# Kernel tuning notes

Measured on AMD Instinct MI355X. Metric: run time of the kernel, lower is better.

Reference implementation:

```python
import jax, jax.numpy as jnp
import numpy as np

N_NODES = 50000

def gcn_conv(x, src, dst, W, b, n_nodes):
    # PyG GCNConv: add self-loops, symmetric normalization D^-1/2 (A+I) D^-1/2, then bias
    loop = jnp.arange(n_nodes)
    s = jnp.concatenate([src, loop])
    d = jnp.concatenate([dst, loop])
    deg = jax.ops.segment_sum(jnp.ones(s.shape[0], x.dtype), d, num_segments=n_nodes)
    dinv = jnp.where(deg > 0, jax.lax.rsqrt(deg), 0.0)
    norm = dinv[s] * dinv[d]                      # [E+N]
    h = x @ W                                      # [N, out]
    msg = h[s] * norm[:, None]                     # gather + scale
    out = jax.ops.segment_sum(msg, d, num_segments=n_nodes)  # scatter-add
    return out + b

def setup_inputs() -> dict:
    key = jax.random.key(0)
    ks = jax.random.split(key, 8)
    x = jax.random.normal(ks[0], (N_NODES, 128), jnp.float32)
    edge_index = jax.random.randint(ks[1], (2, 800000), 0, N_NODES)
    def glorot(k, fan_in, fan_out):
        lim = np.sqrt(6.0 / (fan_in + fan_out)).astype(np.float32)
        return jax.random.uniform(k, (fan_in, fan_out), jnp.float32, -lim, lim)
    return {
        "x": x,
        "edge_index": edge_index,
        "conv_w1": glorot(ks[2], 128, 64), "conv_b1": jnp.zeros((64,), jnp.float32),
        "conv_w2": glorot(ks[3], 64, 64),  "conv_b2": jnp.zeros((64,), jnp.float32),
        "fc_w1": glorot(ks[4], 64, 32),    "fc_b1": jnp.zeros((32,), jnp.float32),
        "fc_w2": glorot(ks[5], 32, 1),     "fc_b2": jnp.zeros((1,), jnp.float32),
    }

def reference(x, edge_index, conv_w1, conv_b1, conv_w2, conv_b2, fc_w1, fc_b1, fc_w2, fc_b2):
    src, dst = edge_index[0], edge_index[1]
    h = jnp.tanh(gcn_conv(x, src, dst, conv_w1, conv_b1, N_NODES))
    h = jnp.tanh(gcn_conv(h, src, dst, conv_w2, conv_b2, N_NODES))
    h = jnp.tanh(h @ fc_w1 + fc_b1)  # dropout is identity at inference
    return h @ fc_w2 + fc_b2          # [N, 1]
```

## Files before the change

kernel.cpp:

```cpp
#include <hip/hip_runtime.h>
#include <math.h>

#define TPB 256
#define NBK_MAX 512
#define CAP 4096
#define FILL_CAP 4096
#define SC_CH 16
#define DMAX 64

typedef short bf16x8 __attribute__((ext_vector_type(8)));
typedef float f32x4 __attribute__((ext_vector_type(4)));

__device__ __forceinline__ unsigned short rne_bf16(float f) {
  unsigned u = __float_as_uint(f);
  return (unsigned short)((u + 0x7fffu + ((u >> 16) & 1u)) >> 16);
}
__device__ __forceinline__ float bf16_f(unsigned short v) {
  return __uint_as_float((unsigned)v << 16);
}
__device__ __forceinline__ float blo(unsigned u) { return __uint_as_float(u << 16); }
__device__ __forceinline__ float bhi(unsigned u) { return __uint_as_float(u & 0xffff0000u); }
__device__ __forceinline__ float ftanh(float x) {
  float xc = fminf(fmaxf(x, -15.f), 15.f);
  float e = __expf(2.f * xc);
  return (e - 1.f) * __builtin_amdgcn_rcpf(e + 1.f);
}

__global__ __launch_bounds__(TPB) void k_init(int* __restrict__ gcur,
                                              unsigned short* __restrict__ hz,
                                              int NBK, int N) {
  int i = blockIdx.x * TPB + threadIdx.x;
  if (i < NBK) gcur[i] = i * CAP;
  if (blockIdx.x == 0 && threadIdx.x < 32)
    ((unsigned*)(hz + ((size_t)N << 6)))[threadIdx.x] = 0;
}

__global__ __launch_bounds__(TPB) void k_bscatter(const int* __restrict__ src,
                                                  const int* __restrict__ dst,
                                                  int* __restrict__ gcur,
                                                  unsigned* __restrict__ e2,
                                                  int E, int NBK) {
  __shared__ int h[NBK_MAX];
  __shared__ int base[NBK_MAX];
  int tid = threadIdx.x, blk = blockIdx.x, G = gridDim.x;
  int chunk = (E + G - 1) / G, lo = blk * chunk, hi = min(E, lo + chunk);
  for (int t0 = lo; t0 < hi; t0 += TPB * SC_CH) {
    int sv[SC_CH], dv[SC_CH];
    for (int b = tid; b < NBK; b += TPB) h[b] = 0;
    __syncthreads();
#pragma unroll
    for (int u = 0; u < SC_CH; ++u) {
      int e = t0 + u * TPB + tid;
      if (e < hi) {
        dv[u] = dst[e];
        sv[u] = src[e];
        atomicAdd(&h[dv[u] >> 7], 1);
      } else {
        dv[u] = -1;
      }
    }
    __syncthreads();
    for (int b = tid; b < NBK; b += TPB) {
      int c = h[b];
      if (c) {
        int o = atomicAdd(&gcur[b], c);
        base[b] = min(o, (b + 1) * CAP - c);
      }
    }
    __syncthreads();
    for (int b = tid; b < NBK; b += TPB) h[b] = 0;
    __syncthreads();
#pragma unroll
    for (int u = 0; u < SC_CH; ++u) {
      if (dv[u] >= 0) {
        int bk = dv[u] >> 7;
        int r = atomicAdd(&h[bk], 1);
        e2[base[bk] + r] = ((unsigned)sv[u] << 7) | (unsigned)(dv[u] & 127);
      }
    }
    __syncthreads();
  }
}

__global__ __launch_bounds__(TPB) void k_build(const unsigned* __restrict__ e2,
                                               const int* __restrict__ gcur,
                                               float* __restrict__ dinv,
                                               int* __restrict__ col2, int N) {
  __shared__ int c[128], sc[128], cur[128];
  __shared__ int buf[FILL_CAP];
  int tid = threadIdx.x, b = blockIdx.x;
  int st = b * CAP;
  int en = min(gcur[b], st + FILL_CAP);
  if (tid < 128) c[tid] = 0;
  __syncthreads();
  for (int i = st + tid; i < en; i += TPB) atomicAdd(&c[e2[i] & 127u], 1);
  __syncthreads();
  if (tid < 128) sc[tid] = c[tid];
  __syncthreads();
  for (int o = 1; o < 128; o <<= 1) {
    int v = (tid >= o && tid < 128) ? sc[tid - o] : 0;
    __syncthreads();
    if (tid < 128) sc[tid] += v;
    __syncthreads();
  }
  if (tid < 128) {
    cur[tid] = sc[tid] - c[tid];
    int node = b * 128 + tid;
    if (node < N) dinv[node] = rsqrtf((float)(c[tid] + 1));
  }
  __syncthreads();
  for (int i = st + tid; i < en; i += TPB) {
    unsigned v = e2[i];
    int p = atomicAdd(&cur[v & 127u], 1);
    buf[p] = (int)(v >> 7);
  }
  __syncthreads();
  for (int i = tid; i < 128 * DMAX; i += TPB) {
    int nl = i >> 6, k = i & 63;
    int node = b * 128 + nl;
    if (node < N) {
      int cc = c[nl];
      int v;
      if (k == 0) v = node;
      else if (k - 1 < cc) v = buf[sc[nl] - cc + k - 1];
      else v = N;
      col2[((size_t)node << 6) + k] = v;
    }
  }
}

template <int K, bool AF32>
__global__ __launch_bounds__(TPB) void k_mm(const void* __restrict__ Ap,
                                            const float* __restrict__ W,
                                            const float* __restrict__ dinv,
                                            unsigned short* __restrict__ Hout, int N) {
  constexpr int P = K + 8;
  __shared__ unsigned short sHi[64 * P];
  __shared__ unsigned short sLo[64 * P];
  int tid = threadIdx.x;
  for (int i = tid; i < K * 64; i += TPB) {
    int k = i >> 6, n = i & 63;
    float w = W[i];
    unsigned short hb = rne_bf16(w);
    sHi[n * P + k] = hb;
    sLo[n * P + k] = rne_bf16(w - bf16_f(hb));
  }
  __syncthreads();
  int wave = tid >> 6, lane = tid & 63;
  int oct = lane >> 4, l15 = lane & 15;
  int base = blockIdx.x * 64 + wave * 16;
  int arow = base + l15;
  if (arow >= N) arow = N - 1;
  f32x4 acc[4] = {};
#pragma unroll
  for (int s = 0; s < K / 32; ++s) {
    bf16x8 ahi, alo;
    if (AF32) {
      const float* ap = (const float*)Ap + (size_t)arow * K + s * 32 + oct * 8;
      float4 f0 = *(const float4*)ap;
      float4 f1 = *(const float4*)(ap + 4);
      float fv[8] = {f0.x, f0.y, f0.z, f0.w, f1.x, f1.y, f1.z, f1.w};
#pragma unroll
      for (int j = 0; j < 8; ++j) {
        unsigned short hb = rne_bf16(fv[j]);
        ahi[j] = (short)hb;
        alo[j] = (short)rne_bf16(fv[j] - bf16_f(hb));
      }
    } else {
      ahi = *(const bf16x8*)((const unsigned short*)Ap + (size_t)arow * K + s * 32 + oct * 8);
    }
#pragma unroll
    for (int t = 0; t < 4; ++t) {
      bf16x8 bh = *(const bf16x8*)(sHi + (t * 16 + l15) * P + s * 32 + oct * 8);
      bf16x8 bl = *(const bf16x8*)(sLo + (t * 16 + l15) * P + s * 32 + oct * 8);
      acc[t] = __builtin_amdgcn_mfma_f32_16x16x32_bf16(ahi, bh, acc[t], 0, 0, 0);
      acc[t] = __builtin_amdgcn_mfma_f32_16x16x32_bf16(ahi, bl, acc[t], 0, 0, 0);
      if (AF32)
        acc[t] = __builtin_amdgcn_mfma_f32_16x16x32_bf16(alo, bh, acc[t], 0, 0, 0);
    }
  }
#pragma unroll
  for (int r = 0; r < 4; ++r) {
    int row = base + oct * 4 + r;
    if (row < N) {
      float dv = dinv[row];
#pragma unroll
      for (int t = 0; t < 4; ++t)
        Hout[(size_t)row * 64 + t * 16 + l15] = rne_bf16(acc[t][r] * dv);
    }
  }
}


#define AQ_ISSUE(J, HVS)                                                        \
  {                                                                             \
    _Pragma("unroll") for (int g = 0; g < 8; ++g) {                             \
      int s0 = __builtin_amdgcn_readlane(sv[J], g);                             \
      int s1 = __builtin_amdgcn_readlane(sv[J], 8 + g);                         \
      int s = half ? s1 : s0;                                                   \
      HVS[0][g] = *(const unsigned*)(H + ((size_t)s << 6) + f2 * 2);            \
    }                                                                           \
    if (cnt[J] > 16) {                                                          \
      _Pragma("unroll") for (int g = 0; g < 8; ++g) {                           \
        int s0 = __builtin_amdgcn_readlane(sv[J], 16 + g);                      \
        int s1 = __builtin_amdgcn_readlane(sv[J], 24 + g);                      \
        int s = half ? s1 : s0;                                                 \
        HVS[1][g] = *(const unsigned*)(H + ((size_t)s << 6) + f2 * 2);          \
      }                                                                         \
    }                                                                           \
  }

#define AQ_ACC(J, HVS)                                                          \
  {                                                                             \
    float x = 0.f, y = 0.f;                                                     \
    _Pragma("unroll") for (int g = 0; g < 8; ++g) {                             \
      x += blo(HVS[0][g]);                                                      \
      y += bhi(HVS[0][g]);                                                      \
    }                                                                           \
    if (cnt[J] > 16) {                                                          \
      _Pragma("unroll") for (int g = 0; g < 8; ++g) {                           \
        x += blo(HVS[1][g]);                                                    \
        y += bhi(HVS[1][g]);                                                    \
      }                                                                         \
      for (int t = 32; t < cnt[J]; t += 16) {              \
        unsigned tv[8];                                                         \
        _Pragma("unroll") for (int g = 0; g < 8; ++g) {                         \
          int s0 = __builtin_amdgcn_readlane(sv[J], t + g);                     \
          int s1 = __builtin_amdgcn_readlane(sv[J], t + 8 + g);                 \
          int s = half ? s1 : s0;                                               \
          tv[g] = *(const unsigned*)(H + ((size_t)s << 6) + f2 * 2);            \
        }                                                                       \
        _Pragma("unroll") for (int g = 0; g < 8; ++g) {                         \
          x += blo(tv[g]);                                                      \
          y += bhi(tv[g]);                                                      \
        }                                                                       \
      }                                                                         \
    }                                                                           \
    x += __shfl_xor(x, 32);                                                     \
    y += __shfl_xor(y, 32);                                                     \
    float di_ = rsqrtf((float)cnt[J]);                                          \
    float yx_ = ftanh(di_ * x + bf.x);                                          \
    float yy_ = ftanh(di_ * y + bf.y);                                          \
    if constexpr (DOFC) {                                                       \
      if (half == 0) {                                                          \
        float* sp_ = sA + ((wid << 3) + (J)) * 64 + f2 * 2;                     \
        sp_[0] = yx_;                                                           \
        sp_[1] = yy_;                                                           \
      }                                                                         \
    } else {                                                                    \
      if (half == 0 && qb + (J) < N) {                                          \
        unsigned pk_ = (unsigned)rne_bf16(yx_) | ((unsigned)rne_bf16(yy_) << 16); \
        ((unsigned*)OUT)[((size_t)(qb + (J)) << 5) + f2] = pk_;                 \
      }                                                                         \
    }                                                                           \
  }

template <bool DOFC>
__global__ __launch_bounds__(TPB) void k_agg(const unsigned short* __restrict__ H,
                                             const int* __restrict__ col2,
                                             const float* __restrict__ bias,
                                             unsigned short* __restrict__ OUT,
                                             const float* __restrict__ fw1,
                                             const float* __restrict__ fb1,
                                             const float* __restrict__ fw2,
                                             const float* __restrict__ fb2,
                                             float* __restrict__ fout, int N) {
  __shared__ float sw1t[DOFC ? 32 * 66 : 1];
  __shared__ float sb1[DOFC ? 32 : 1];
  __shared__ float sw2[DOFC ? 32 : 1];
  __shared__ float sA[DOFC ? 4 * 8 * 64 : 1];
  int tid = threadIdx.x;
  int wid = tid >> 6, lane = tid & 63;
  int f2 = lane & 31, half = lane >> 5;
  float b2v = 0.f;
  if constexpr (DOFC) {
    for (int i = tid; i < 32 * 64; i += TPB) {
      int j = i >> 6, k = i & 63;
      sw1t[j * 66 + k] = fw1[k * 32 + j];
    }
    if (tid < 32) { sb1[tid] = fb1[tid]; sw2[tid] = fw2[tid]; }
    b2v = fb2[0];
    __syncthreads();
  }
  float2 bf = *(const float2*)(bias + f2 * 2);

  int qb = (blockIdx.x * 4 + wid) * 8;
  if (qb >= N) return;

  int idx[8];
#pragma unroll
  for (int j = 0; j < 8; ++j) idx[j] = min(qb + j, N - 1);
  int sv[8];
#pragma unroll
  for (int j = 0; j < 8; ++j) sv[j] = col2[((size_t)idx[j] << 6) + lane];
  int cnt[8];
#pragma unroll
  for (int j = 0; j < 8; ++j) {
    unsigned long long mb_ = __ballot(sv[j] != N);
    cnt[j] = __builtin_amdgcn_readfirstlane((int)__popcll(mb_));
  }
  unsigned hvA[2][8], hvB[2][8];
  AQ_ISSUE(0, hvA)
  AQ_ISSUE(1, hvB)
  AQ_ACC(0, hvA)
  AQ_ISSUE(2, hvA)
  AQ_ACC(1, hvB)
  AQ_ISSUE(3, hvB)
  AQ_ACC(2, hvA)
  AQ_ISSUE(4, hvA)
  AQ_ACC(3, hvB)
  AQ_ISSUE(5, hvB)
  AQ_ACC(4, hvA)
  AQ_ISSUE(6, hvA)
  AQ_ACC(5, hvB)
  AQ_ISSUE(7, hvB)
  AQ_ACC(6, hvA)
  AQ_ACC(7, hvB)

  if constexpr (DOFC) {
    int m = lane & 31;
#pragma unroll
    for (int p = 0; p < 4; ++p) {
      int nl = p * 2 + half;
      int node = qb + nl;
      float acc = sb1[m];
      const float2* ar = (const float2*)(sA + ((wid << 3) + nl) * 64);
      const float2* wr = (const float2*)(sw1t + m * 66);
#pragma unroll
      for (int k2 = 0; k2 < 32; ++k2) {
        float2 av = ar[k2];
        float2 wv = wr[k2];
        acc += av.x * wv.x + av.y * wv.y;
      }
      float t = ftanh(acc) * sw2[m];
#pragma unroll
      for (int o = 1; o < 32; o <<= 1) t += __shfl_xor(t, o);
      if (m == 0 && node < N) fout[node] = t + b2v;
    }
  }
}


extern "C" void kernel_launch(void* const* d_in, const int* in_sizes, int n_in,
                              void* d_out, int out_size, void* d_ws, size_t ws_size,
                              hipStream_t stream) {
  const float* x   = (const float*)d_in[0];
  const int*   ei  = (const int*)d_in[1];
  const float* w1  = (const float*)d_in[2];
  const float* b1  = (const float*)d_in[3];
  const float* w2  = (const float*)d_in[4];
  const float* b2  = (const float*)d_in[5];
  const float* fw1 = (const float*)d_in[6];
  const float* fb1 = (const float*)d_in[7];
  const float* fw2 = (const float*)d_in[8];
  const float* fb2 = (const float*)d_in[9];
  float* out = (float*)d_out;

  int N = in_sizes[0] / 128;
  int E = in_sizes[1] / 2;
  const int* src = ei;
  const int* dst = ei + E;

  const int G   = 256;
  const int NBK = (N + 127) / 128;

  char* p = (char*)d_ws;
  size_t off = 0;
  auto take = [&](size_t bytes) -> void* {
    void* r = p + off;
    off += (bytes + 255) & ~(size_t)255;
    return r;
  };
  int*            gcur = (int*)take((size_t)NBK * 4);
  float*          dinv = (float*)take((size_t)N * 4);
  unsigned*       e2   = (unsigned*)take((size_t)NBK * CAP * 4);
  int*            col2 = (int*)take((size_t)N * DMAX * 4);
  unsigned short* h    = (unsigned short*)take((size_t)(N + 1) * 64 * 2);
  unsigned short* a    = (unsigned short*)take((size_t)N * 64 * 2);
  (void)ws_size; (void)n_in; (void)out_size;

  k_init<<<(NBK + TPB - 1) / TPB, TPB, 0, stream>>>(gcur, h, NBK, N);
  k_bscatter<<<G, TPB, 0, stream>>>(src, dst, gcur, e2, E, NBK);
  k_build<<<NBK, TPB, 0, stream>>>(e2, gcur, dinv, col2, N);

  int gmm = (N + 63) / 64;
  int gagg = (N + 31) / 32;
  k_mm<128, true><<<gmm, TPB, 0, stream>>>(x, w1, dinv, h, N);
  k_agg<false><<<gagg, TPB, 0, stream>>>(h, col2, b1, a,
                                         nullptr, nullptr, nullptr, nullptr,
                                         nullptr, N);
  k_mm<64, false><<<gmm, TPB, 0, stream>>>(a, w2, dinv, h, N);
  k_agg<true><<<gagg, TPB, 0, stream>>>(h, col2, b2, nullptr,
                                        fw1, fb1, fw2, fb2, out, N);
}
```

Before: 188.5 us.

## Store padded adjacency as 16-bit indices and always issue second gather batch

The padded per-node neighbor table is stored as unsigned short instead of int, halving its write traffic in k_build and its read traffic in both aggregation passes, with k_build writing two packed indices per 32-bit store. The gather macros use 32-bit byte offsets from a char base pointer instead of size_t index arithmetic, and the second batch of 16 neighbor loads is issued unconditionally, which removes branches but adds loads of the padding row for low-degree nodes. This relies on N fitting in 16 bits, which holds for 50000 nodes with the sentinel N.

```diff
diff --git a/kernel.cpp b/kernel.cpp
--- a/kernel.cpp
+++ b/kernel.cpp
@@ -85,7 +85,7 @@
 __global__ __launch_bounds__(TPB) void k_build(const unsigned* __restrict__ e2,
                                                const int* __restrict__ gcur,
                                                float* __restrict__ dinv,
-                                               int* __restrict__ col2, int N) {
+                                               unsigned short* __restrict__ col2, int N) {
   __shared__ int c[128], sc[128], cur[128];
   __shared__ int buf[FILL_CAP];
   int tid = threadIdx.x, b = blockIdx.x;
@@ -115,16 +115,16 @@
     buf[p] = (int)(v >> 7);
   }
   __syncthreads();
-  for (int i = tid; i < 128 * DMAX; i += TPB) {
-    int nl = i >> 6, k = i & 63;
+  for (int i = tid; i < 128 * 32; i += TPB) {
+    int nl = i >> 5, kk = i & 31;
     int node = b * 128 + nl;
     if (node < N) {
-      int cc = c[nl];
-      int v;
-      if (k == 0) v = node;
-      else if (k - 1 < cc) v = buf[sc[nl] - cc + k - 1];
-      else v = N;
-      col2[((size_t)node << 6) + k] = v;
+      int cc = c[nl], base0 = sc[nl] - cc;
+      int k0 = kk * 2, k1 = kk * 2 + 1;
+      unsigned v0 = (k0 == 0) ? (unsigned)node
+                              : ((k0 - 1 < cc) ? (unsigned)buf[base0 + k0 - 1] : (unsigned)N);
+      unsigned v1 = (k1 - 1 < cc) ? (unsigned)buf[base0 + k1 - 1] : (unsigned)N;
+      ((unsigned*)col2)[((size_t)node << 5) + kk] = v0 | (v1 << 16);
     }
   }
 }
@@ -197,16 +197,14 @@
     _Pragma("unroll") for (int g = 0; g < 8; ++g) {                             \
       int s0 = __builtin_amdgcn_readlane(sv[J], g);                             \
       int s1 = __builtin_amdgcn_readlane(sv[J], 8 + g);                         \
-      int s = half ? s1 : s0;                                                   \
-      HVS[0][g] = *(const unsigned*)(H + ((size_t)s << 6) + f2 * 2);            \
-    }                                                                           \
-    if (cnt[J] > 16) {                                                          \
-      _Pragma("unroll") for (int g = 0; g < 8; ++g) {                           \
-        int s0 = __builtin_amdgcn_readlane(sv[J], 16 + g);                      \
-        int s1 = __builtin_amdgcn_readlane(sv[J], 24 + g);                      \
-        int s = half ? s1 : s0;                                                 \
-        HVS[1][g] = *(const unsigned*)(H + ((size_t)s << 6) + f2 * 2);          \
-      }                                                                         \
+      unsigned off0 = ((unsigned)(half ? s1 : s0) << 7) + foff;                 \
+      HVS[0][g] = *(const unsigned*)(Hb + off0);                                \
+    }                                                                           \
+    _Pragma("unroll") for (int g = 0; g < 8; ++g) {                             \
+      int s0 = __builtin_amdgcn_readlane(sv[J], 16 + g);                        \
+      int s1 = __builtin_amdgcn_readlane(sv[J], 24 + g);                        \
+      unsigned off1 = ((unsigned)(half ? s1 : s0) << 7) + foff;                 \
+      HVS[1][g] = *(const unsigned*)(Hb + off1);                                \
     }                                                                           \
   }
 
@@ -217,18 +215,18 @@
       x += blo(HVS[0][g]);                                                      \
       y += bhi(HVS[0][g]);                                                      \
     }                                                                           \
-    if (cnt[J] > 16) {                                                          \
-      _Pragma("unroll") for (int g = 0; g < 8; ++g) {                           \
-        x += blo(HVS[1][g]);                                                    \
-        y += bhi(HVS[1][g]);                                                    \
-      }                                                                         \
-      for (int t = 32; t < cnt[J]; t += 16) {              \
+    _Pragma("unroll") for (int g = 0; g < 8; ++g) {                             \
+      x += blo(HVS[1][g]);                                                      \
+      y += bhi(HVS[1][g]);                                                      \
+    }                                                                           \
+    if (cnt[J] > 32) {                \
+      for (int t = 32; t < cnt[J]; t += 16) {                                   \
         unsigned tv[8];                                                         \
         _Pragma("unroll") for (int g = 0; g < 8; ++g) {                         \
           int s0 = __builtin_amdgcn_readlane(sv[J], t + g);                     \
           int s1 = __builtin_amdgcn_readlane(sv[J], t + 8 + g);                 \
-          int s = half ? s1 : s0;                                               \
-          tv[g] = *(const unsigned*)(H + ((size_t)s << 6) + f2 * 2);            \
+          unsigned offt = ((unsigned)(half ? s1 : s0) << 7) + foff;             \
+          tv[g] = *(const unsigned*)(Hb + offt);                                \
         }                                                                       \
         _Pragma("unroll") for (int g = 0; g < 8; ++g) {                         \
           x += blo(tv[g]);                                                      \
@@ -257,7 +255,7 @@
 
 template <bool DOFC>
 __global__ __launch_bounds__(TPB) void k_agg(const unsigned short* __restrict__ H,
-                                             const int* __restrict__ col2,
+                                             const unsigned short* __restrict__ col2,
                                              const float* __restrict__ bias,
                                              unsigned short* __restrict__ OUT,
                                              const float* __restrict__ fw1,
@@ -283,6 +281,8 @@
     __syncthreads();
   }
   float2 bf = *(const float2*)(bias + f2 * 2);
+  const char* Hb = (const char*)H;
+  unsigned foff = (unsigned)(f2 * 4);
 
   int qb = (blockIdx.x * 4 + wid) * 8;
   if (qb >= N) return;
@@ -292,7 +292,7 @@
   for (int j = 0; j < 8; ++j) idx[j] = min(qb + j, N - 1);
   int sv[8];
 #pragma unroll
-  for (int j = 0; j < 8; ++j) sv[j] = col2[((size_t)idx[j] << 6) + lane];
+  for (int j = 0; j < 8; ++j) sv[j] = (int)col2[((size_t)idx[j] << 6) + lane];
   int cnt[8];
 #pragma unroll
   for (int j = 0; j < 8; ++j) {
@@ -374,7 +374,7 @@
   int*            gcur = (int*)take((size_t)NBK * 4);
   float*          dinv = (float*)take((size_t)N * 4);
   unsigned*       e2   = (unsigned*)take((size_t)NBK * CAP * 4);
-  int*            col2 = (int*)take((size_t)N * DMAX * 4);
+  unsigned short* col2 = (unsigned short*)take((size_t)N * DMAX * 2);
   unsigned short* h    = (unsigned short*)take((size_t)(N + 1) * 64 * 2);
   unsigned short* a    = (unsigned short*)take((size_t)N * 64 * 2);
   (void)ws_size; (void)n_in; (void)out_size;
```

After: 183.1 us. -2.9%, faster.
